# Kernel tuning notes

Hardware: AMD Instinct MI355X
Metric: run time of the kernel (lower is better)

Reference implementation:

```python
import jax, jax.numpy as jnp
import numpy as np

B, N = 32, 1024
NUM = B * N
DIMS = [(1, 128, 8), (128, 128, 8), (128, 64, 16), (64, 64, 16), (64, 32, 1)]  # (cin, cout, heads)

def _edges():
    # bidirectional chain per batch element, offset by N per graph (as in torch forward)
    a = np.arange(N - 1)
    offs = (np.arange(B) * N)[:, None]
    src = np.concatenate([(a[None] + offs).ravel(), (a[None] + 1 + offs).ravel()])
    dst = np.concatenate([(a[None] + 1 + offs).ravel(), (a[None] + offs).ravel()])
    return jnp.asarray(src, jnp.int32), jnp.asarray(dst, jnp.int32)

def _conv(x, src, dst, Wm, bm, Ws, bs, att):
    # PyG GeneralConv: directed msg, additive attention, aggr='add', head-mean, + lin_self
    h, cout = att.shape
    m = (x @ Wm + bm)[src].reshape(-1, h, cout)          # [E, H, C] edge messages
    m = jnp.where(m > 0, m, 0.01 * m)                    # F.leaky_relu default slope 0.01
    alpha = jnp.einsum('ehc,hc->eh', m, att)             # [E, H] attention logits
    amax = jax.ops.segment_max(alpha, dst, num_segments=NUM)
    ex = jnp.exp(alpha - amax[dst])
    den = jax.ops.segment_sum(ex, dst, num_segments=NUM)
    w = ex / (den[dst] + 1e-16)                          # segment softmax over incoming edges
    agg = jax.ops.segment_sum(m * w[:, :, None], dst, num_segments=NUM)  # [NUM, H, C]
    return agg.mean(axis=1) + x @ Ws + bs                # head mean + self loop linear

def _forward(nodes, params, Wc, bc):
    src, dst = _edges()
    x = nodes.reshape(NUM, 1)
    for i, p in enumerate(params):
        x = _conv(x, src, dst, *p)
        if i < 4:
            x = jax.nn.elu(x)                            # Dropout(0.4) identity at eval
    out = x.reshape(B, N, -1)[:, -1, :]                  # last node per graph -> [B, 32]
    return out @ Wc + bc, out

def setup_inputs():
    key = jax.random.key(0)
    ks = jax.random.split(key, 20)
    inp = {"nodes": jax.random.normal(ks[0], (B, N), dtype=jnp.float32)}
    i = 1
    for l, (cin, cout, h) in enumerate(DIMS, 1):
        s = float(1.0 / np.sqrt(cin))
        inp["Wm%d" % l] = jax.random.uniform(ks[i], (cin, h * cout), jnp.float32, -s, s); i += 1
        inp["bm%d" % l] = jnp.zeros((h * cout,), jnp.float32)
        inp["Ws%d" % l] = jax.random.uniform(ks[i], (cin, cout), jnp.float32, -s, s); i += 1
        inp["bs%d" % l] = jnp.zeros((cout,), jnp.float32)
        inp["att%d" % l] = jax.random.normal(ks[i], (h, cout), jnp.float32) * 0.1; i += 1
    inp["Wc"] = jax.random.normal(ks[i], (32, 1), jnp.float32) * 0.1
    inp["bc"] = jnp.zeros((1,), jnp.float32)
    return inp

def reference(nodes, Wm1, bm1, Ws1, bs1, att1, Wm2, bm2, Ws2, bs2, att2, Wm3, bm3, Ws3, bs3, att3, Wm4, bm4, Ws4, bs4, att4, Wm5, bm5, Ws5, bs5, att5, Wc, bc):
    params = [(Wm1, bm1, Ws1, bs1, att1), (Wm2, bm2, Ws2, bs2, att2), (Wm3, bm3, Ws3, bs3, att3), (Wm4, bm4, Ws4, bs4, att4), (Wm5, bm5, Ws5, bs5, att5)]
    return _forward(nodes, params, Wc, bc)
```

## Files before the change

kernel.cpp:

```cpp
#include <hip/hip_runtime.h>

#define BATCH 32
#define NLEN  1024
#define NUMV  (BATCH * NLEN)

typedef __attribute__((ext_vector_type(8))) short short8;
typedef __attribute__((ext_vector_type(4))) float f32x4;

__device__ inline unsigned short rne_bf16(float x) {
    union { float f; unsigned u; } a; a.f = x;
    return (unsigned short)((a.u + 0x7FFFu + ((a.u >> 16) & 1u)) >> 16);
}
__device__ inline void bsplit(float x, unsigned short& h, unsigned short& l) {
    union { float f; unsigned u; } a; a.f = x;
    unsigned hb = (a.u + 0x7FFFu + ((a.u >> 16) & 1u)) & 0xFFFF0000u;
    h = (unsigned short)(hb >> 16);
    union { unsigned u; float f; } hf; hf.u = hb;
    l = rne_bf16(x - hf.f);
}
__device__ inline float bf16_to_f(unsigned short v) {
    union { unsigned u; float f; } a; a.u = ((unsigned)v) << 16; return a.f;
}

template<int CIN, int COUT, int H>
__device__ void pack_layer(const float* __restrict__ Wm, const float* __restrict__ Ws,
                           unsigned short* __restrict__ out, int t0, int nthr)
{
    constexpr int HC = H * COUT;
    constexpr int KC = ((CIN + 31) & ~31) / 32;
    constexpr int NT = (HC + COUT) / 16;
    const int total = NT * KC * 1024;
    for (int f = t0; f < total; f += nthr) {
        int j = f & 7, g = (f >> 3) & 3, c = (f >> 5) & 15, hl = (f >> 9) & 1;
        int r2 = f >> 10;
        int kc = r2 % KC, nt = r2 / KC;
        int k = kc * 32 + g * 8 + j, col = nt * 16 + c;
        float v = 0.f;
        if (k < CIN) v = (col < HC) ? Wm[k * HC + col] : Ws[k * COUT + (col - HC)];
        unsigned short h, l; bsplit(v, h, l);
        out[f] = hl ? l : h;
    }
}

__global__ void pack_all(const float* Wm1, const float* Ws1, const float* Wm2, const float* Ws2,
                         const float* Wm3, const float* Ws3, const float* Wm4, const float* Ws4,
                         unsigned short* p1, unsigned short* p2, unsigned short* p3, unsigned short* p4)
{
    int t = blockIdx.x * 256 + threadIdx.x;
    int n = gridDim.x * 256;
    pack_layer<1, 128, 8>(Wm1, Ws1, p1, t, n);
    pack_layer<128, 128, 8>(Wm2, Ws2, p2, t, n);
    pack_layer<128, 64, 16>(Wm3, Ws3, p3, t, n);
    pack_layer<64, 64, 16>(Wm4, Ws4, p4, t, n);
}

template<int CIN, int COUT, int H, bool MPACK>
__global__ __launch_bounds__(256, 2)
void conv_reg(const float* __restrict__ x, const unsigned short* __restrict__ pw,
              const float* __restrict__ bm, const float* __restrict__ bs,
              const float* __restrict__ att, float* __restrict__ y)
{
    constexpr int HC = H * COUT;
    static_assert(HC == 1024, "");
    constexpr int KC   = ((CIN + 31) & ~31) / 32;
    constexpr int HT   = COUT / 16;
    constexpr int MT   = HC / 16;
    constexpr int NTOT = MT + HT;
    constexpr int NCH  = KC * 128;
    constexpr int CHPT = (NCH + 255) / 256;
    constexpr int ROWSB = 112;
    constexpr int TPG  = (NLEN + ROWSB - 1) / ROWSB;
    constexpr float invH = 1.0f / H;

    const int tid  = threadIdx.x;
    const int lane = tid & 63;
    const int w    = tid >> 6;
    const int r    = lane & 15;
    const int gg   = lane >> 4;
    const int g    = blockIdx.x / TPG;
    const int n0   = (blockIdx.x % TPG) * ROWSB;
    const size_t gstart = (size_t)g * NLEN;

    __shared__ alignas(16) unsigned short bufs[2][KC * 1024];

    short8 a_hi[2][KC], a_lo[2][KC];
    #pragma unroll
    for (int s = 0; s < 2; s++) {
        const int na = n0 - 1 + w * 28 + s * 14 + r;
        const bool av = (na >= 0) && (na < NLEN);
        const float* xrow = x + (gstart + (size_t)(av ? na : 0)) * CIN;
        #pragma unroll
        for (int kc = 0; kc < KC; kc++) {
            float vals[8];
            if constexpr (CIN % 32 == 0) {
                if (av) {
                    f32x4 v0 = *(const f32x4*)(xrow + kc * 32 + gg * 8);
                    f32x4 v1 = *(const f32x4*)(xrow + kc * 32 + gg * 8 + 4);
                    vals[0]=v0[0]; vals[1]=v0[1]; vals[2]=v0[2]; vals[3]=v0[3];
                    vals[4]=v1[0]; vals[5]=v1[1]; vals[6]=v1[2]; vals[7]=v1[3];
                } else {
                    #pragma unroll
                    for (int jj = 0; jj < 8; jj++) vals[jj] = 0.f;
                }
            } else {
                #pragma unroll
                for (int jj = 0; jj < 8; jj++) {
                    int k = kc * 32 + gg * 8 + jj;
                    vals[jj] = (av && k < CIN) ? xrow[k] : 0.f;
                }
            }
            union { short8 v; unsigned short u[8]; } hu, lu;
            #pragma unroll
            for (int jj = 0; jj < 8; jj++) bsplit(vals[jj], hu.u[jj], lu.u[jj]);
            a_hi[s][kc] = hu.v; a_lo[s][kc] = lu.v;
        }
    }

    float out[2][HT][4];
    #pragma unroll
    for (int s = 0; s < 2; s++)
        #pragma unroll
        for (int q = 0; q < HT; q++)
            #pragma unroll
            for (int e = 0; e < 4; e++) out[s][q][e] = 0.f;

    float    mf[2][MPACK ? 1 : HT][4];
    unsigned mpk[2][MPACK ? HT : 1][2];

    {
        const f32x4* ps = (const f32x4*)pw;
        f32x4 sreg[CHPT];
        #pragma unroll
        for (int i = 0; i < CHPT; i++) { int idx = tid + i * 256; if (idx < NCH) sreg[i] = ps[idx]; }
        #pragma unroll
        for (int i = 0; i < CHPT; i++) { int idx = tid + i * 256; if (idx < NCH) *(f32x4*)&bufs[0][idx * 8] = sreg[i]; }
    }
    __syncthreads();

    for (int h = 0; h < H; h++) {
        float p[2][4] = {{0.f,0.f,0.f,0.f},{0.f,0.f,0.f,0.f}};
        #pragma unroll
        for (int q = 0; q < HT; q++) {
            const int nt  = h * HT + q;
            const int cur = nt & 1;
            const int ntn = nt + 1;
            const bool doStage = (ntn < NTOT);
            f32x4 sreg[CHPT];
            if (doStage) {
                const f32x4* ps = (const f32x4*)pw + (size_t)ntn * NCH;
                #pragma unroll
                for (int i = 0; i < CHPT; i++) { int idx = tid + i * 256; if (idx < NCH) sreg[i] = ps[idx]; }
            }
            const int boff = r * 32 + gg * 8;
            const int col  = nt * 16 + r;
            const float bmv  = bm[col];
            const float attv = att[col];
            short8 bh[KC], bl[KC];
            #pragma unroll
            for (int kc = 0; kc < KC; kc++) {
                bh[kc] = *(const short8*)&bufs[cur][(kc * 2 + 0) * 512 + boff];
                bl[kc] = *(const short8*)&bufs[cur][(kc * 2 + 1) * 512 + boff];
            }
            #pragma unroll
            for (int s = 0; s < 2; s++) {
                f32x4 acc = {bmv, bmv, bmv, bmv};
                #pragma unroll
                for (int kc = 0; kc < KC; kc++) {
                    acc = __builtin_amdgcn_mfma_f32_16x16x32_bf16(a_hi[s][kc], bh[kc], acc, 0, 0, 0);
                    acc = __builtin_amdgcn_mfma_f32_16x16x32_bf16(a_hi[s][kc], bl[kc], acc, 0, 0, 0);
                    acc = __builtin_amdgcn_mfma_f32_16x16x32_bf16(a_lo[s][kc], bh[kc], acc, 0, 0, 0);
                }
                float vv[4];
                #pragma unroll
                for (int e = 0; e < 4; e++) {
                    float v = acc[e];
                    v = v > 0.f ? v : 0.01f * v;
                    vv[e] = v;
                    p[s][e] += v * attv;
                }
                if constexpr (MPACK) {
                    mpk[s][q][0] = ((unsigned)rne_bf16(vv[1]) << 16) | rne_bf16(vv[0]);
                    mpk[s][q][1] = ((unsigned)rne_bf16(vv[3]) << 16) | rne_bf16(vv[2]);
                } else {
                    #pragma unroll
                    for (int e = 0; e < 4; e++) mf[s][q][e] = vv[e];
                }
            }
            if (doStage) {
                const int nb = ntn & 1;
                #pragma unroll
                for (int i = 0; i < CHPT; i++) { int idx = tid + i * 256; if (idx < NCH) *(f32x4*)&bufs[nb][idx * 8] = sreg[i]; }
            }
            __syncthreads();
        }
        #pragma unroll
        for (int s = 0; s < 2; s++)
            #pragma unroll
            for (int e = 0; e < 4; e++) {
                float v = p[s][e];
                v += __shfl_xor(v, 1, 64);
                v += __shfl_xor(v, 2, 64);
                v += __shfl_xor(v, 4, 64);
                v += __shfl_xor(v, 8, 64);
                p[s][e] = v;
            }
        #pragma unroll
        for (int s = 0; s < 2; s++) {
            const int jbase = w * 28 + s * 14;
            float a3u = __shfl_up(p[s][3], 16, 64);
            float a0d = __shfl_down(p[s][0], 16, 64);
            float wpv[4], wnv[4];
            #pragma unroll
            for (int e = 0; e < 4; e++) {
                const int jr = gg * 4 + e;
                const int nl = n0 - 1 + jbase + jr;
                const bool hp = nl >= 1;
                const bool hn = nl < NLEN - 1;
                float ap = (e > 0) ? p[s][e - 1] : a3u;
                float an = (e < 3) ? p[s][e + 1] : a0d;
                float apx = hp ? ap : -1e30f;
                float anx = hn ? an : -1e30f;
                float mx = fmaxf(apx, anx);
                float ep = hp ? __expf(ap - mx) : 0.f;
                float en = hn ? __expf(an - mx) : 0.f;
                float inv = 1.f / (ep + en + 1e-16f);
                wpv[e] = ep * inv; wnv[e] = en * inv;
            }
            #pragma unroll
            for (int q = 0; q < HT; q++) {
                float v0, v1, v2, v3;
                if constexpr (MPACK) {
                    v0 = bf16_to_f((unsigned short)(mpk[s][q][0] & 0xffff));
                    v1 = bf16_to_f((unsigned short)(mpk[s][q][0] >> 16));
                    v2 = bf16_to_f((unsigned short)(mpk[s][q][1] & 0xffff));
                    v3 = bf16_to_f((unsigned short)(mpk[s][q][1] >> 16));
                } else {
                    v0 = mf[s][q][0]; v1 = mf[s][q][1]; v2 = mf[s][q][2]; v3 = mf[s][q][3];
                }
                float m3u = __shfl_up(v3, 16, 64);
                float m0d = __shfl_down(v0, 16, 64);
                float mvals[4] = {v0, v1, v2, v3};
                #pragma unroll
                for (int e = 0; e < 4; e++) {
                    float mprev = (e > 0) ? mvals[e - 1] : m3u;
                    float mnext = (e < 3) ? mvals[e + 1] : m0d;
                    out[s][q][e] += wpv[e] * mprev + wnv[e] * mnext;
                }
            }
        }
    }

    #pragma unroll
    for (int q2 = 0; q2 < HT; q2++) {
        const int nt  = MT + q2;
        const int cur = nt & 1;
        const int ntn = nt + 1;
        const bool doStage = (ntn < NTOT);
        f32x4 sreg[CHPT];
        if (doStage) {
            const f32x4* ps = (const f32x4*)pw + (size_t)ntn * NCH;
            #pragma unroll
            for (int i = 0; i < CHPT; i++) { int idx = tid + i * 256; if (idx < NCH) sreg[i] = ps[idx]; }
        }
        const int boff = r * 32 + gg * 8;
        const int c2   = q2 * 16 + r;
        const float bsv = bs[c2];
        short8 bh[KC], bl[KC];
        #pragma unroll
        for (int kc = 0; kc < KC; kc++) {
            bh[kc] = *(const short8*)&bufs[cur][(kc * 2 + 0) * 512 + boff];
            bl[kc] = *(const short8*)&bufs[cur][(kc * 2 + 1) * 512 + boff];
        }
        #pragma unroll
        for (int s = 0; s < 2; s++) {
            f32x4 acc = {bsv, bsv, bsv, bsv};
            #pragma unroll
            for (int kc = 0; kc < KC; kc++) {
                acc = __builtin_amdgcn_mfma_f32_16x16x32_bf16(a_hi[s][kc], bh[kc], acc, 0, 0, 0);
                acc = __builtin_amdgcn_mfma_f32_16x16x32_bf16(a_hi[s][kc], bl[kc], acc, 0, 0, 0);
                acc = __builtin_amdgcn_mfma_f32_16x16x32_bf16(a_lo[s][kc], bh[kc], acc, 0, 0, 0);
            }
            const int jbase = w * 28 + s * 14;
            #pragma unroll
            for (int e = 0; e < 4; e++) {
                const int jr = gg * 4 + e;
                const int nl = n0 - 1 + jbase + jr;
                float v = out[s][q2][e] * invH + acc[e];
                v = v > 0.f ? v : __expf(v) - 1.f;
                if (jr >= 1 && jr <= 14 && nl < NLEN)
                    y[(gstart + nl) * COUT + c2] = v;
            }
        }
        if (doStage) {
            const int nb = ntn & 1;
            #pragma unroll
            for (int i = 0; i < CHPT; i++) { int idx = tid + i * 256; if (idx < NCH) *(f32x4*)&bufs[nb][idx * 8] = sreg[i]; }
        }
        __syncthreads();
    }
}

__global__ void final_head(const float* __restrict__ x4,
                           const float* __restrict__ Wm,
                           const float* __restrict__ bm,
                           const float* __restrict__ Ws,
                           const float* __restrict__ bs,
                           const float* __restrict__ Wc,
                           const float* __restrict__ bc,
                           float* __restrict__ out)
{
    int g = blockIdx.x;
    int c = threadIdx.x;
    const float* xu = &x4[((long)g * NLEN + NLEN - 2) * 64];
    const float* xv = xu + 64;
    float o = 0.f;
    if (c < 32) {
        float m = bm[c];
        float s = bs[c];
        for (int k = 0; k < 64; k++) {
            m = fmaf(xu[k], Wm[k * 32 + c], m);
            s = fmaf(xv[k], Ws[k * 32 + c], s);
        }
        m = m > 0.f ? m : 0.01f * m;
        o = m + s;
        out[32 + g * 32 + c] = o;
    }
    float tsum = (c < 32) ? o * Wc[c] : 0.f;
    #pragma unroll
    for (int sft = 16; sft > 0; sft >>= 1)
        tsum += __shfl_xor(tsum, sft, 64);
    if (c == 0) out[g] = tsum + bc[0];
}

extern "C" void kernel_launch(void* const* d_in, const int* in_sizes, int n_in,
                              void* d_out, int out_size, void* d_ws, size_t ws_size,
                              hipStream_t stream)
{
    const float* nodes = (const float*)d_in[0];
    auto L = [&](int l, int k) { return (const float*)d_in[1 + (l - 1) * 5 + k]; };

    float* xb0 = (float*)d_ws;
    float* xb1 = xb0 + (size_t)NUMV * 128;
    unsigned short* p1 = (unsigned short*)(xb1 + (size_t)NUMV * 128);
    unsigned short* p2 = p1 + 72 * 1024;
    unsigned short* p3 = p2 + 72 * 4096;
    unsigned short* p4 = p3 + 68 * 4096;

    pack_all<<<dim3(512), dim3(256), 0, stream>>>(
        L(1,0), L(1,2), L(2,0), L(2,2), L(3,0), L(3,2), L(4,0), L(4,2), p1, p2, p3, p4);

    constexpr int TPG = (NLEN + 111) / 112;
    dim3 grid(BATCH * TPG);
    dim3 blk(256);

    conv_reg<1,   128, 8,  false><<<grid, blk, 0, stream>>>(nodes, p1, L(1,1), L(1,3), L(1,4), xb0);
    conv_reg<128, 128, 8,  true ><<<grid, blk, 0, stream>>>(xb0,   p2, L(2,1), L(2,3), L(2,4), xb1);
    conv_reg<128, 64,  16, false><<<grid, blk, 0, stream>>>(xb1,   p3, L(3,1), L(3,3), L(3,4), xb0);
    conv_reg<64,  64,  16, false><<<grid, blk, 0, stream>>>(xb0,   p4, L(4,1), L(4,3), L(4,4), xb1);

    final_head<<<dim3(BATCH), dim3(64), 0, stream>>>(
        xb1, L(5,0), L(5,1), L(5,2), L(5,3),
        (const float*)d_in[26], (const float*)d_in[27], (float*)d_out);
}
```

Measured before the change: 401.3 us.

## Halve rows per block, drop dual sub-tile, permute weight pack for conflict-free LDS reads

Measured after the change: 341.7 us. -14.9%, faster.

```diff
diff --git a/kernel.cpp b/kernel.cpp
--- a/kernel.cpp
+++ b/kernel.cpp
@@ -31,7 +31,10 @@
     constexpr int NT = (HC + COUT) / 16;
     const int total = NT * KC * 1024;
     for (int f = t0; f < total; f += nthr) {
-        int j = f & 7, g = (f >> 3) & 3, c = (f >> 5) & 15, hl = (f >> 9) & 1;
+        int j  = f & 7;
+        int c  = (f >> 3) & 15;
+        int g  = (f >> 7) & 3;
+        int hl = (f >> 9) & 1;
         int r2 = f >> 10;
         int kc = r2 % KC, nt = r2 / KC;
         int k = kc * 32 + g * 8 + j, col = nt * 16 + c;
@@ -55,7 +58,7 @@
 }
 
 template<int CIN, int COUT, int H, bool MPACK>
-__global__ __launch_bounds__(256, 2)
+__global__ __launch_bounds__(256, 3)
 void conv_reg(const float* __restrict__ x, const unsigned short* __restrict__ pw,
               const float* __restrict__ bm, const float* __restrict__ bs,
               const float* __restrict__ att, float* __restrict__ y)
@@ -68,7 +71,7 @@
     constexpr int NTOT = MT + HT;
     constexpr int NCH  = KC * 128;
     constexpr int CHPT = (NCH + 255) / 256;
-    constexpr int ROWSB = 112;
+    constexpr int ROWSB = 56;
     constexpr int TPG  = (NLEN + ROWSB - 1) / ROWSB;
     constexpr float invH = 1.0f / H;
 
@@ -83,10 +86,9 @@
 
     __shared__ alignas(16) unsigned short bufs[2][KC * 1024];
 
-    short8 a_hi[2][KC], a_lo[2][KC];
-    #pragma unroll
-    for (int s = 0; s < 2; s++) {
-        const int na = n0 - 1 + w * 28 + s * 14 + r;
+    short8 a_hi[KC], a_lo[KC];
+    {
+        const int na = n0 - 1 + w * 14 + r;
         const bool av = (na >= 0) && (na < NLEN);
         const float* xrow = x + (gstart + (size_t)(av ? na : 0)) * CIN;
         #pragma unroll
@@ -112,20 +114,18 @@
             union { short8 v; unsigned short u[8]; } hu, lu;
             #pragma unroll
             for (int jj = 0; jj < 8; jj++) bsplit(vals[jj], hu.u[jj], lu.u[jj]);
-            a_hi[s][kc] = hu.v; a_lo[s][kc] = lu.v;
-        }
-    }
-
-    float out[2][HT][4];
+            a_hi[kc] = hu.v; a_lo[kc] = lu.v;
+        }
+    }
+
+    float out[HT][4];
     #pragma unroll
-    for (int s = 0; s < 2; s++)
-        #pragma unroll
-        for (int q = 0; q < HT; q++)
-            #pragma unroll
-            for (int e = 0; e < 4; e++) out[s][q][e] = 0.f;
-
-    float    mf[2][MPACK ? 1 : HT][4];
-    unsigned mpk[2][MPACK ? HT : 1][2];
+    for (int q = 0; q < HT; q++)
+        #pragma unroll
+        for (int e = 0; e < 4; e++) out[q][e] = 0.f;
+
+    float    mf[MPACK ? 1 : HT][4];
+    unsigned mpk[MPACK ? HT : 1][2];
 
     {
         const f32x4* ps = (const f32x4*)pw;
@@ -137,8 +137,10 @@
     }
     __syncthreads();
 
+    const int boff = gg * 128 + r * 8;
+
     for (int h = 0; h < H; h++) {
-        float p[2][4] = {{0.f,0.f,0.f,0.f},{0.f,0.f,0.f,0.f}};
+        float p[4] = {0.f, 0.f, 0.f, 0.f};
         #pragma unroll
         for (int q = 0; q < HT; q++) {
             const int nt  = h * HT + q;
@@ -151,7 +153,6 @@
                 #pragma unroll
                 for (int i = 0; i < CHPT; i++) { int idx = tid + i * 256; if (idx < NCH) sreg[i] = ps[idx]; }
             }
-            const int boff = r * 32 + gg * 8;
             const int col  = nt * 16 + r;
             const float bmv  = bm[col];
             const float attv = att[col];
@@ -161,30 +162,27 @@
                 bh[kc] = *(const short8*)&bufs[cur][(kc * 2 + 0) * 512 + boff];
                 bl[kc] = *(const short8*)&bufs[cur][(kc * 2 + 1) * 512 + boff];
             }
-            #pragma unroll
-            for (int s = 0; s < 2; s++) {
-                f32x4 acc = {bmv, bmv, bmv, bmv};
-                #pragma unroll
-                for (int kc = 0; kc < KC; kc++) {
-                    acc = __builtin_amdgcn_mfma_f32_16x16x32_bf16(a_hi[s][kc], bh[kc], acc, 0, 0, 0);
-                    acc = __builtin_amdgcn_mfma_f32_16x16x32_bf16(a_hi[s][kc], bl[kc], acc, 0, 0, 0);
-                    acc = __builtin_amdgcn_mfma_f32_16x16x32_bf16(a_lo[s][kc], bh[kc], acc, 0, 0, 0);
-                }
-                float vv[4];
-                #pragma unroll
-                for (int e = 0; e < 4; e++) {
-                    float v = acc[e];
-                    v = v > 0.f ? v : 0.01f * v;
-                    vv[e] = v;
-                    p[s][e] += v * attv;
-                }
-                if constexpr (MPACK) {
-                    mpk[s][q][0] = ((unsigned)rne_bf16(vv[1]) << 16) | rne_bf16(vv[0]);
-                    mpk[s][q][1] = ((unsigned)rne_bf16(vv[3]) << 16) | rne_bf16(vv[2]);
-                } else {
-                    #pragma unroll
-                    for (int e = 0; e < 4; e++) mf[s][q][e] = vv[e];
-                }
+            f32x4 acc = {bmv, bmv, bmv, bmv};
+            #pragma unroll
+            for (int kc = 0; kc < KC; kc++) {
+                acc = __builtin_amdgcn_mfma_f32_16x16x32_bf16(a_hi[kc], bh[kc], acc, 0, 0, 0);
+                acc = __builtin_amdgcn_mfma_f32_16x16x32_bf16(a_hi[kc], bl[kc], acc, 0, 0, 0);
+                acc = __builtin_amdgcn_mfma_f32_16x16x32_bf16(a_lo[kc], bh[kc], acc, 0, 0, 0);
+            }
+            float vv[4];
+            #pragma unroll
+            for (int e = 0; e < 4; e++) {
+                float v = acc[e];
+                v = v > 0.f ? v : 0.01f * v;
+                vv[e] = v;
+                p[e] += v * attv;
+            }
+            if constexpr (MPACK) {
+                mpk[q][0] = ((unsigned)rne_bf16(vv[1]) << 16) | rne_bf16(vv[0]);
+                mpk[q][1] = ((unsigned)rne_bf16(vv[3]) << 16) | rne_bf16(vv[2]);
+            } else {
+                #pragma unroll
+                for (int e = 0; e < 4; e++) mf[q][e] = vv[e];
             }
             if (doStage) {
                 const int nb = ntn & 1;
@@ -194,21 +192,18 @@
             __syncthreads();
         }
         #pragma unroll
-        for (int s = 0; s < 2; s++)
-            #pragma unroll
-            for (int e = 0; e < 4; e++) {
-                float v = p[s][e];
-                v += __shfl_xor(v, 1, 64);
-                v += __shfl_xor(v, 2, 64);
-                v += __shfl_xor(v, 4, 64);
-                v += __shfl_xor(v, 8, 64);
-                p[s][e] = v;
-            }
-        #pragma unroll
-        for (int s = 0; s < 2; s++) {
-            const int jbase = w * 28 + s * 14;
-            float a3u = __shfl_up(p[s][3], 16, 64);
-            float a0d = __shfl_down(p[s][0], 16, 64);
+        for (int e = 0; e < 4; e++) {
+            float v = p[e];
+            v += __shfl_xor(v, 1, 64);
+            v += __shfl_xor(v, 2, 64);
+            v += __shfl_xor(v, 4, 64);
+            v += __shfl_xor(v, 8, 64);
+            p[e] = v;
+        }
+        {
+            const int jbase = w * 14;
+            float a3u = __shfl_up(p[3], 16, 64);
+            float a0d = __shfl_down(p[0], 16, 64);
             float wpv[4], wnv[4];
             #pragma unroll
             for (int e = 0; e < 4; e++) {
@@ -216,8 +211,8 @@
                 const int nl = n0 - 1 + jbase + jr;
                 const bool hp = nl >= 1;
                 const bool hn = nl < NLEN - 1;
-                float ap = (e > 0) ? p[s][e - 1] : a3u;
-                float an = (e < 3) ? p[s][e + 1] : a0d;
+                float ap = (e > 0) ? p[e - 1] : a3u;
+                float an = (e < 3) ? p[e + 1] : a0d;
                 float apx = hp ? ap : -1e30f;
                 float anx = hn ? an : -1e30f;
                 float mx = fmaxf(apx, anx);
@@ -230,12 +225,12 @@
             for (int q = 0; q < HT; q++) {
                 float v0, v1, v2, v3;
                 if constexpr (MPACK) {
-                    v0 = bf16_to_f((unsigned short)(mpk[s][q][0] & 0xffff));
-                    v1 = bf16_to_f((unsigned short)(mpk[s][q][0] >> 16));
-                    v2 = bf16_to_f((unsigned short)(mpk[s][q][1] & 0xffff));
-                    v3 = bf16_to_f((unsigned short)(mpk[s][q][1] >> 16));
+                    v0 = bf16_to_f((unsigned short)(mpk[q][0] & 0xffff));
+                    v1 = bf16_to_f((unsigned short)(mpk[q][0] >> 16));
+                    v2 = bf16_to_f((unsigned short)(mpk[q][1] & 0xffff));
+                    v3 = bf16_to_f((unsigned short)(mpk[q][1] >> 16));
                 } else {
-                    v0 = mf[s][q][0]; v1 = mf[s][q][1]; v2 = mf[s][q][2]; v3 = mf[s][q][3];
+                    v0 = mf[q][0]; v1 = mf[q][1]; v2 = mf[q][2]; v3 = mf[q][3];
                 }
                 float m3u = __shfl_up(v3, 16, 64);
                 float m0d = __shfl_down(v0, 16, 64);
@@ -244,7 +239,7 @@
                 for (int e = 0; e < 4; e++) {
                     float mprev = (e > 0) ? mvals[e - 1] : m3u;
                     float mnext = (e < 3) ? mvals[e + 1] : m0d;
-                    out[s][q][e] += wpv[e] * mprev + wnv[e] * mnext;
+                    out[q][e] += wpv[e] * mprev + wnv[e] * mnext;
                 }
             }
         }
@@ -262,8 +257,7 @@
             #pragma unroll
             for (int i = 0; i < CHPT; i++) { int idx = tid + i * 256; if (idx < NCH) sreg[i] = ps[idx]; }
         }
-        const int boff = r * 32 + gg * 8;
-        const int c2   = q2 * 16 + r;
+        const int c2  = q2 * 16 + r;
         const float bsv = bs[c2];
         short8 bh[KC], bl[KC];
         #pragma unroll
@@ -271,25 +265,22 @@
             bh[kc] = *(const short8*)&bufs[cur][(kc * 2 + 0) * 512 + boff];
             bl[kc] = *(const short8*)&bufs[cur][(kc * 2 + 1) * 512 + boff];
         }
-        #pragma unroll
-        for (int s = 0; s < 2; s++) {
-            f32x4 acc = {bsv, bsv, bsv, bsv};
-            #pragma unroll
-            for (int kc = 0; kc < KC; kc++) {
-                acc = __builtin_amdgcn_mfma_f32_16x16x32_bf16(a_hi[s][kc], bh[kc], acc, 0, 0, 0);
-                acc = __builtin_amdgcn_mfma_f32_16x16x32_bf16(a_hi[s][kc], bl[kc], acc, 0, 0, 0);
-                acc = __builtin_amdgcn_mfma_f32_16x16x32_bf16(a_lo[s][kc], bh[kc], acc, 0, 0, 0);
-            }
-            const int jbase = w * 28 + s * 14;
-            #pragma unroll
-            for (int e = 0; e < 4; e++) {
-                const int jr = gg * 4 + e;
-                const int nl = n0 - 1 + jbase + jr;
-                float v = out[s][q2][e] * invH + acc[e];
-                v = v > 0.f ? v : __expf(v) - 1.f;
-                if (jr >= 1 && jr <= 14 && nl < NLEN)
-                    y[(gstart + nl) * COUT + c2] = v;
-            }
+        f32x4 acc = {bsv, bsv, bsv, bsv};
+        #pragma unroll
+        for (int kc = 0; kc < KC; kc++) {
+            acc = __builtin_amdgcn_mfma_f32_16x16x32_bf16(a_hi[kc], bh[kc], acc, 0, 0, 0);
+            acc = __builtin_amdgcn_mfma_f32_16x16x32_bf16(a_hi[kc], bl[kc], acc, 0, 0, 0);
+            acc = __builtin_amdgcn_mfma_f32_16x16x32_bf16(a_lo[kc], bh[kc], acc, 0, 0, 0);
+        }
+        const int jbase = w * 14;
+        #pragma unroll
+        for (int e = 0; e < 4; e++) {
+            const int jr = gg * 4 + e;
+            const int nl = n0 - 1 + jbase + jr;
+            float v = out[q2][e] * invH + acc[e];
+            v = v > 0.f ? v : __expf(v) - 1.f;
+            if (jr >= 1 && jr <= 14 && nl < NLEN)
+                y[(gstart + nl) * COUT + c2] = v;
         }
         if (doStage) {
             const int nb = ntn & 1;
@@ -349,7 +340,7 @@
     pack_all<<<dim3(512), dim3(256), 0, stream>>>(
         L(1,0), L(1,2), L(2,0), L(2,2), L(3,0), L(3,2), L(4,0), L(4,2), p1, p2, p3, p4);
 
-    constexpr int TPG = (NLEN + 111) / 112;
+    constexpr int TPG = (NLEN + 55) / 56;
     dim3 grid(BATCH * TPG);
     dim3 blk(256);
 
```
